# Kernel optimization log

Hardware: AMD Instinct MI355X
Metric: run time of the kernel (lower is better)

## Reference

```python
import jax, jax.numpy as jnp
import numpy as np

HEAD_SIZE = 64
N_EMBD = 768

def setup_inputs() -> dict:
    key = jax.random.key(0)
    kx, kq, kk, kv = jax.random.split(key, 4)
    x = jax.random.normal(kx, (4, 4096, N_EMBD), dtype=jnp.float32)
    s = 1.0 / np.sqrt(N_EMBD)
    Wq = jax.random.normal(kq, (N_EMBD, HEAD_SIZE), dtype=jnp.float32) * s
    Wk = jax.random.normal(kk, (N_EMBD, HEAD_SIZE), dtype=jnp.float32) * s
    Wv = jax.random.normal(kv, (N_EMBD, HEAD_SIZE), dtype=jnp.float32) * s
    return {"x": x, "Wq": Wq, "Wk": Wk, "Wv": Wv}

def reference(x, Wq, Wk, Wv):
    b, t, c = x.shape
    h = Wq.shape[1]
    q = jnp.einsum('btc,ch->bth', x, Wq)
    k = jnp.einsum('btc,ch->bth', x, Wk)
    v = jnp.einsum('btc,ch->bth', x, Wv)
    scores = jnp.einsum('bqh,bkh->bqk', q, k) / jnp.sqrt(jnp.float32(h))
    causal = jnp.tril(jnp.ones((t, t), dtype=bool))  # [t,t]
    scores = jnp.where(causal, scores, -jnp.inf)
    attn = jax.nn.softmax(scores, axis=-1)
    return jnp.einsum('bqk,bkh->bqh', attn, v)
```

## Files before the change

kernel.cpp:

```cpp
#include <hip/hip_runtime.h>
#include <math.h>

#define BB 4
#define TT 4096
#define CC 768
#define HH 64
#define NN 192
#define LDP 72
#define GR 32
#define BKK 64

typedef __bf16 bf16x8 __attribute__((ext_vector_type(8)));
typedef float floatx4 __attribute__((ext_vector_type(4)));
typedef unsigned short u16x8 __attribute__((ext_vector_type(8)));

__device__ inline unsigned short f2bf(float f) {
    union { __bf16 b; unsigned short u; } v;
    v.b = (__bf16)f;
    return v.u;
}

__global__ __launch_bounds__(256) void wprep(const float* __restrict__ Wq,
                                             const float* __restrict__ Wk,
                                             const float* __restrict__ Wv,
                                             unsigned short* __restrict__ wtf) {
    const int idx = blockIdx.x * 256 + threadIdx.x;
    if (idx >= NN * CC) return;
    const int j = idx & 7;
    const int lane = (idx >> 3) & 63;
    const int rest = idx >> 9;
    const int kg = rest % 24;
    const int n_tile = rest / 24;
    const int c = kg * 32 + (lane >> 4) * 8 + j;
    const int n = n_tile * 16 + (lane & 15);
    const float* W = (n < 64) ? Wq : (n < 128) ? Wk : Wv;
    wtf[idx] = f2bf(W[c * HH + (n & 63)]);
}

__global__ __launch_bounds__(256) void qkv_gemm(const float* __restrict__ x,
                                                const unsigned short* __restrict__ wtf,
                                                unsigned short* __restrict__ qb,
                                                unsigned short* __restrict__ kb,
                                                unsigned short* __restrict__ vbt) {
    __shared__ unsigned short As[GR * LDP];

    const int tid = threadIdx.x;
    const int w = tid >> 6, lane = tid & 63;
    const int l15 = lane & 15, quad = lane >> 4;
    const int m0 = blockIdx.x * GR;
    const int n0 = w * 48;
    const int nt0 = w * 3;

    const int ar = tid >> 3;
    const int akoff = (tid & 7) * 8;
    const float* xp = x + (size_t)(m0 + ar) * CC + akoff;

    floatx4 acc[2][3] = {};

    float4 pa0 = *(const float4*)(xp);
    float4 pa1 = *(const float4*)(xp + 4);

    for (int step = 0; step < 12; ++step) {
        __syncthreads();
        u16x8 pk;
        pk[0] = f2bf(pa0.x); pk[1] = f2bf(pa0.y);
        pk[2] = f2bf(pa0.z); pk[3] = f2bf(pa0.w);
        pk[4] = f2bf(pa1.x); pk[5] = f2bf(pa1.y);
        pk[6] = f2bf(pa1.z); pk[7] = f2bf(pa1.w);
        *(u16x8*)(As + ar * LDP + akoff) = pk;
        __syncthreads();

        if (step < 11) {
            pa0 = *(const float4*)(xp + (step + 1) * BKK);
            pa1 = *(const float4*)(xp + (step + 1) * BKK + 4);
        }

        bf16x8 a0[2], a1[2];
#pragma unroll
        for (int rg = 0; rg < 2; ++rg) {
            a0[rg] = *(const bf16x8*)(As + (16 * rg + l15) * LDP + quad * 8);
            a1[rg] = *(const bf16x8*)(As + (16 * rg + l15) * LDP + 32 + quad * 8);
        }
#pragma unroll
        for (int j = 0; j < 3; ++j) {
            const unsigned short* bp =
                wtf + ((size_t)((nt0 + j) * 24 + 2 * step) * 64 + lane) * 8;
            const bf16x8 b0 = *(const bf16x8*)(bp);
            const bf16x8 b1 = *(const bf16x8*)(bp + 512);
#pragma unroll
            for (int rg = 0; rg < 2; ++rg) {
                acc[rg][j] = __builtin_amdgcn_mfma_f32_16x16x32_bf16(a0[rg], b0, acc[rg][j], 0, 0, 0);
                acc[rg][j] = __builtin_amdgcn_mfma_f32_16x16x32_bf16(a1[rg], b1, acc[rg][j], 0, 0, 0);
            }
        }
    }

    const int b = m0 >> 12;
#pragma unroll
    for (int j = 0; j < 3; ++j) {
        const int n = n0 + j * 16 + l15;
        const int mid = n >> 6;
        const int h = n & 63;
#pragma unroll
        for (int rg = 0; rg < 2; ++rg) {
            const int tloc = (m0 & (TT - 1)) + 16 * rg + quad * 4;
            if (mid == 2) {
                ushort4 pk;
                pk.x = f2bf(acc[rg][j][0]); pk.y = f2bf(acc[rg][j][1]);
                pk.z = f2bf(acc[rg][j][2]); pk.w = f2bf(acc[rg][j][3]);
                *(ushort4*)(vbt + ((size_t)b * HH + h) * TT + tloc) = pk;
            } else {
                unsigned short* dst = (mid == 0) ? qb : kb;
#pragma unroll
                for (int r = 0; r < 4; ++r)
                    dst[(size_t)(m0 + 16 * rg + quad * 4 + r) * HH + h] = f2bf(acc[rg][j][r]);
            }
        }
    }
}

template<int CH>
__global__ __launch_bounds__(256) void attn_part(const unsigned short* __restrict__ qb,
                                                 const unsigned short* __restrict__ kb,
                                                 const unsigned short* __restrict__ vbt,
                                                 float* __restrict__ Opart,
                                                 float* __restrict__ lsum) {
    __shared__ unsigned short Ks[64 * LDP];
    __shared__ unsigned short VTs[64 * LDP];
    __shared__ unsigned short Ps[4][16 * LDP];

    constexpr int NG = 64 / CH;
    constexpr int TOTB = CH * (NG * (NG + 1)) / 2;

    const int b = blockIdx.x & 3;
    int rem = TOTB - 1 - (blockIdx.x >> 2);
    int g = 0;
    while (rem >= CH * (g + 1)) { rem -= CH * (g + 1); ++g; }
    const int qt = g * CH + rem / (g + 1);
    const int ch = rem - (rem / (g + 1)) * (g + 1);

    const int q0  = qt * 64;
    const int tid = threadIdx.x;
    const int w = tid >> 6, lane = tid & 63;
    const int l15 = lane & 15, quad = lane >> 4;

    const unsigned short* Qb  = qb  + (size_t)b * TT * HH;
    const unsigned short* Kb  = kb  + (size_t)b * TT * HH;
    const unsigned short* VTb = vbt + (size_t)b * HH * TT;

    const int qrow = q0 + 16 * w + l15;
    const bf16x8 qf0 = *(const bf16x8*)(Qb + (size_t)qrow * HH + quad * 8);
    const bf16x8 qf1 = *(const bf16x8*)(Qb + (size_t)qrow * HH + 32 + quad * 8);

    floatx4 O[4] = {};
    floatx4 lacc = {0.f, 0.f, 0.f, 0.f};

    const int kt0 = ch * CH;
    const int kt1 = min(kt0 + CH, qt + 1);
    for (int kt = kt0; kt < kt1; ++kt) {
        __syncthreads();
        const unsigned short* Kt = Kb + (size_t)(kt * 64) * HH;
        const unsigned short* Vt = VTb + kt * 64;
#pragma unroll
        for (int e = 0; e < 2; ++e) {
            const int chunk = tid + 256 * e;
            const int r = chunk >> 3, c0 = (chunk & 7) * 8;
            *(u16x8*)(Ks + r * LDP + c0)  = *(const u16x8*)(Kt + r * HH + c0);
            *(u16x8*)(VTs + r * LDP + c0) = *(const u16x8*)(Vt + (size_t)r * TT + c0);
        }
        __syncthreads();

        floatx4 s[4];
#pragma unroll
        for (int ki = 0; ki < 4; ++ki) {
            const bf16x8 kf0 = *(const bf16x8*)(Ks + (16 * ki + l15) * LDP + quad * 8);
            const bf16x8 kf1 = *(const bf16x8*)(Ks + (16 * ki + l15) * LDP + 32 + quad * 8);
            floatx4 c = {};
            c = __builtin_amdgcn_mfma_f32_16x16x32_bf16(qf0, kf0, c, 0, 0, 0);
            c = __builtin_amdgcn_mfma_f32_16x16x32_bf16(qf1, kf1, c, 0, 0, 0);
            s[ki] = c * 0.125f;
        }

        if (kt == qt) {
#pragma unroll
            for (int ki = 0; ki < 4; ++ki)
#pragma unroll
                for (int r = 0; r < 4; ++r) {
                    const int kloc = 16 * ki + l15;
                    const int qloc = 16 * w + quad * 4 + r;
                    if (kloc > qloc) s[ki][r] = -INFINITY;
                }
        }

#pragma unroll
        for (int ki = 0; ki < 4; ++ki)
#pragma unroll
            for (int r = 0; r < 4; ++r) {
                const float p = __expf(s[ki][r]);
                s[ki][r] = p;
                lacc[r] += p;
            }

        unsigned short* Pw = Ps[w];
#pragma unroll
        for (int ki = 0; ki < 4; ++ki)
#pragma unroll
            for (int r = 0; r < 4; ++r)
                Pw[(quad * 4 + r) * LDP + 16 * ki + l15] = f2bf(s[ki][r]);

        const bf16x8 pf0 = *(const bf16x8*)(Pw + l15 * LDP + quad * 8);
        const bf16x8 pf1 = *(const bf16x8*)(Pw + l15 * LDP + 32 + quad * 8);
#pragma unroll
        for (int di = 0; di < 4; ++di) {
            const bf16x8 vf0 = *(const bf16x8*)(VTs + (16 * di + l15) * LDP + quad * 8);
            const bf16x8 vf1 = *(const bf16x8*)(VTs + (16 * di + l15) * LDP + 32 + quad * 8);
            O[di] = __builtin_amdgcn_mfma_f32_16x16x32_bf16(pf0, vf0, O[di], 0, 0, 0);
            O[di] = __builtin_amdgcn_mfma_f32_16x16x32_bf16(pf1, vf1, O[di], 0, 0, 0);
        }
    }

    float l_r[4];
#pragma unroll
    for (int r = 0; r < 4; ++r) {
        float v = lacc[r];
#pragma unroll
        for (int msk = 8; msk >= 1; msk >>= 1) v += __shfl_xor(v, msk, 64);
        l_r[r] = v;
    }

    const int pbase = ((b * 64 + qt) * NG + ch) * 64;
    float* Op = Opart + (size_t)pbase * HH + 16 * w * HH;
#pragma unroll
    for (int di = 0; di < 4; ++di)
#pragma unroll
        for (int r = 0; r < 4; ++r)
            Op[(quad * 4 + r) * HH + 16 * di + l15] = O[di][r];
    if (l15 == 0) {
#pragma unroll
        for (int r = 0; r < 4; ++r)
            lsum[pbase + 16 * w + quad * 4 + r] = l_r[r];
    }
}

template<int CH>
__global__ __launch_bounds__(256) void attn_merge(const float* __restrict__ Opart,
                                                  const float* __restrict__ lsum,
                                                  float* __restrict__ out) {
    constexpr int NG = 64 / CH;
    const int g = blockIdx.x * 256 + threadIdx.x;
    const int row = g >> 6, d = g & 63;
    const int b = row >> 12, t = row & (TT - 1);
    const int qt = t >> 6, rloc = t & 63;
    const int nchunk = qt / CH + 1;
    const int pbase = ((b * 64 + qt) * NG) * 64 + rloc;

    float O = 0.f, L = 0.f;
#pragma unroll 4
    for (int c = 0; c < nchunk; ++c) {
        const int idx = pbase + c * 64;
        L += lsum[idx];
        O += Opart[(size_t)idx * HH + d];
    }
    out[(size_t)row * HH + d] = O / L;
}

__global__ __launch_bounds__(256) void attn_full(const unsigned short* __restrict__ qb,
                                                 const unsigned short* __restrict__ kb,
                                                 const unsigned short* __restrict__ vbt,
                                                 float* __restrict__ out) {
    __shared__ unsigned short Ks[64 * LDP];
    __shared__ unsigned short VTs[64 * LDP];
    __shared__ unsigned short Ps[4][16 * LDP];

    const int b   = blockIdx.x >> 6;
    const int qt  = blockIdx.x & 63;
    const int q0  = qt * 64;
    const int tid = threadIdx.x;
    const int w = tid >> 6, lane = tid & 63;
    const int l15 = lane & 15, quad = lane >> 4;

    const unsigned short* Qb  = qb  + (size_t)b * TT * HH;
    const unsigned short* Kb  = kb  + (size_t)b * TT * HH;
    const unsigned short* VTb = vbt + (size_t)b * HH * TT;

    const int qrow = q0 + 16 * w + l15;
    const bf16x8 qf0 = *(const bf16x8*)(Qb + (size_t)qrow * HH + quad * 8);
    const bf16x8 qf1 = *(const bf16x8*)(Qb + (size_t)qrow * HH + 32 + quad * 8);

    floatx4 O[4] = {};
    floatx4 lacc = {0.f, 0.f, 0.f, 0.f};

    for (int kt = 0; kt <= qt; ++kt) {
        __syncthreads();
        const unsigned short* Kt = Kb + (size_t)(kt * 64) * HH;
        const unsigned short* Vt = VTb + kt * 64;
#pragma unroll
        for (int e = 0; e < 2; ++e) {
            const int chunk = tid + 256 * e;
            const int r = chunk >> 3, c0 = (chunk & 7) * 8;
            *(u16x8*)(Ks + r * LDP + c0)  = *(const u16x8*)(Kt + r * HH + c0);
            *(u16x8*)(VTs + r * LDP + c0) = *(const u16x8*)(Vt + (size_t)r * TT + c0);
        }
        __syncthreads();

        floatx4 s[4];
#pragma unroll
        for (int ki = 0; ki < 4; ++ki) {
            const bf16x8 kf0 = *(const bf16x8*)(Ks + (16 * ki + l15) * LDP + quad * 8);
            const bf16x8 kf1 = *(const bf16x8*)(Ks + (16 * ki + l15) * LDP + 32 + quad * 8);
            floatx4 c = {};
            c = __builtin_amdgcn_mfma_f32_16x16x32_bf16(qf0, kf0, c, 0, 0, 0);
            c = __builtin_amdgcn_mfma_f32_16x16x32_bf16(qf1, kf1, c, 0, 0, 0);
            s[ki] = c * 0.125f;
        }
        if (kt == qt) {
#pragma unroll
            for (int ki = 0; ki < 4; ++ki)
#pragma unroll
                for (int r = 0; r < 4; ++r)
                    if (16 * ki + l15 > 16 * w + quad * 4 + r) s[ki][r] = -INFINITY;
        }
#pragma unroll
        for (int ki = 0; ki < 4; ++ki)
#pragma unroll
            for (int r = 0; r < 4; ++r) {
                const float p = __expf(s[ki][r]);
                s[ki][r] = p; lacc[r] += p;
            }

        unsigned short* Pw = Ps[w];
#pragma unroll
        for (int ki = 0; ki < 4; ++ki)
#pragma unroll
            for (int r = 0; r < 4; ++r)
                Pw[(quad * 4 + r) * LDP + 16 * ki + l15] = f2bf(s[ki][r]);

        const bf16x8 pf0 = *(const bf16x8*)(Pw + l15 * LDP + quad * 8);
        const bf16x8 pf1 = *(const bf16x8*)(Pw + l15 * LDP + 32 + quad * 8);
#pragma unroll
        for (int di = 0; di < 4; ++di) {
            const bf16x8 vf0 = *(const bf16x8*)(VTs + (16 * di + l15) * LDP + quad * 8);
            const bf16x8 vf1 = *(const bf16x8*)(VTs + (16 * di + l15) * LDP + 32 + quad * 8);
            O[di] = __builtin_amdgcn_mfma_f32_16x16x32_bf16(pf0, vf0, O[di], 0, 0, 0);
            O[di] = __builtin_amdgcn_mfma_f32_16x16x32_bf16(pf1, vf1, O[di], 0, 0, 0);
        }
    }
    float l_r[4];
#pragma unroll
    for (int r = 0; r < 4; ++r) {
        float v = lacc[r];
#pragma unroll
        for (int msk = 8; msk >= 1; msk >>= 1) v += __shfl_xor(v, msk, 64);
        l_r[r] = v;
    }
    float* outp = out + ((size_t)b * TT + q0 + 16 * w) * HH;
#pragma unroll
    for (int di = 0; di < 4; ++di)
#pragma unroll
        for (int r = 0; r < 4; ++r)
            outp[(quad * 4 + r) * HH + 16 * di + l15] = O[di][r] / l_r[r];
}

extern "C" void kernel_launch(void* const* d_in, const int* in_sizes, int n_in,
                              void* d_out, int out_size, void* d_ws, size_t ws_size,
                              hipStream_t stream) {
    const float* x  = (const float*)d_in[0];
    const float* Wq = (const float*)d_in[1];
    const float* Wk = (const float*)d_in[2];
    const float* Wv = (const float*)d_in[3];
    float* out = (float*)d_out;

    const size_t nQKV = (size_t)BB * TT * HH;
    unsigned short* qb  = (unsigned short*)d_ws;
    unsigned short* kb  = qb + nQKV;
    unsigned short* vbt = kb + nQKV;
    unsigned short* wtf = vbt + nQKV;
    float* Opart = (float*)(wtf + (size_t)NN * CC);

    const size_t prows8  = (size_t)BB * 64 * 8 * 64;
    const size_t prows16 = (size_t)BB * 64 * 4 * 64;
    float* lsum8  = Opart + prows8 * HH;
    float* lsum16 = Opart + prows16 * HH;
    const size_t need8  = (size_t)((char*)(lsum8  + prows8)  - (char*)d_ws);
    const size_t need16 = (size_t)((char*)(lsum16 + prows16) - (char*)d_ws);

    wprep<<<(NN * CC + 255) / 256, 256, 0, stream>>>(Wq, Wk, Wv, wtf);
    qkv_gemm<<<(BB * TT) / GR, 256, 0, stream>>>(x, wtf, qb, kb, vbt);
    if (ws_size >= need8) {
        attn_part<8><<<BB * 288, 256, 0, stream>>>(qb, kb, vbt, Opart, lsum8);
        attn_merge<8><<<(BB * TT * HH) / 256, 256, 0, stream>>>(Opart, lsum8, out);
    } else if (ws_size >= need16) {
        attn_part<16><<<BB * 160, 256, 0, stream>>>(qb, kb, vbt, Opart, lsum16);
        attn_merge<16><<<(BB * TT * HH) / 256, 256, 0, stream>>>(Opart, lsum16, out);
    } else {
        attn_full<<<BB * (TT / 64), 256, 0, stream>>>(qb, kb, vbt, out);
    }
}
```

Before: 131.9 us.

## Stage full x rows in LDS, bf16 partials, exp2 softmax, direct-write single-chunk tiles

The QKV GEMM now loads the whole 32x768 x tile into LDS once, so the per-step double sync is gone. Attention partial outputs are stored as bf16 instead of fp32, halving partial traffic. Softmax uses exp2 with the log2e constant folded into the scale. Query tiles that have only one chunk write normalized output directly and skip the merge. The merge kernel is vectorized to 8 elements per thread. In exchange, bf16 partials cost accuracy and the larger LDS footprint may reduce GEMM occupancy.

```diff
diff --git a/kernel.cpp b/kernel.cpp
--- a/kernel.cpp
+++ b/kernel.cpp
@@ -8,7 +8,8 @@
 #define NN 192
 #define LDP 72
 #define GR 32
-#define BKK 64
+#define XSTR 776
+#define SC2 0.180336880f
 
 typedef __bf16 bf16x8 __attribute__((ext_vector_type(8)));
 typedef float floatx4 __attribute__((ext_vector_type(4)));
@@ -18,6 +19,11 @@
     union { __bf16 b; unsigned short u; } v;
     v.b = (__bf16)f;
     return v.u;
+}
+__device__ inline float bf2f(unsigned short u) {
+    union { unsigned int u; float f; } v;
+    v.u = (unsigned int)u << 16;
+    return v.f;
 }
 
 __global__ __launch_bounds__(256) void wprep(const float* __restrict__ Wq,
@@ -42,7 +48,7 @@
                                                 unsigned short* __restrict__ qb,
                                                 unsigned short* __restrict__ kb,
                                                 unsigned short* __restrict__ vbt) {
-    __shared__ unsigned short As[GR * LDP];
+    __shared__ unsigned short As[GR * XSTR];
 
     const int tid = threadIdx.x;
     const int w = tid >> 6, lane = tid & 63;
@@ -51,35 +57,29 @@
     const int n0 = w * 48;
     const int nt0 = w * 3;
 
-    const int ar = tid >> 3;
-    const int akoff = (tid & 7) * 8;
-    const float* xp = x + (size_t)(m0 + ar) * CC + akoff;
+    const float* xbase = x + (size_t)m0 * CC;
+#pragma unroll
+    for (int e = 0; e < 12; ++e) {
+        const int c = tid + 256 * e;
+        const int r = c / 96, off = (c - r * 96) * 8;
+        const float4 v0 = *(const float4*)(xbase + (size_t)c * 8);
+        const float4 v1 = *(const float4*)(xbase + (size_t)c * 8 + 4);
+        u16x8 pk;
+        pk[0] = f2bf(v0.x); pk[1] = f2bf(v0.y); pk[2] = f2bf(v0.z); pk[3] = f2bf(v0.w);
+        pk[4] = f2bf(v1.x); pk[5] = f2bf(v1.y); pk[6] = f2bf(v1.z); pk[7] = f2bf(v1.w);
+        *(u16x8*)(As + r * XSTR + off) = pk;
+    }
+    __syncthreads();
 
     floatx4 acc[2][3] = {};
-
-    float4 pa0 = *(const float4*)(xp);
-    float4 pa1 = *(const float4*)(xp + 4);
-
+#pragma unroll 4
     for (int step = 0; step < 12; ++step) {
-        __syncthreads();
-        u16x8 pk;
-        pk[0] = f2bf(pa0.x); pk[1] = f2bf(pa0.y);
-        pk[2] = f2bf(pa0.z); pk[3] = f2bf(pa0.w);
-        pk[4] = f2bf(pa1.x); pk[5] = f2bf(pa1.y);
-        pk[6] = f2bf(pa1.z); pk[7] = f2bf(pa1.w);
-        *(u16x8*)(As + ar * LDP + akoff) = pk;
-        __syncthreads();
-
-        if (step < 11) {
-            pa0 = *(const float4*)(xp + (step + 1) * BKK);
-            pa1 = *(const float4*)(xp + (step + 1) * BKK + 4);
-        }
-
         bf16x8 a0[2], a1[2];
 #pragma unroll
         for (int rg = 0; rg < 2; ++rg) {
-            a0[rg] = *(const bf16x8*)(As + (16 * rg + l15) * LDP + quad * 8);
-            a1[rg] = *(const bf16x8*)(As + (16 * rg + l15) * LDP + 32 + quad * 8);
+            const unsigned short* ap = As + (16 * rg + l15) * XSTR + step * 64 + quad * 8;
+            a0[rg] = *(const bf16x8*)(ap);
+            a1[rg] = *(const bf16x8*)(ap + 32);
         }
 #pragma unroll
         for (int j = 0; j < 3; ++j) {
@@ -123,8 +123,9 @@
 __global__ __launch_bounds__(256) void attn_part(const unsigned short* __restrict__ qb,
                                                  const unsigned short* __restrict__ kb,
                                                  const unsigned short* __restrict__ vbt,
-                                                 float* __restrict__ Opart,
-                                                 float* __restrict__ lsum) {
+                                                 unsigned short* __restrict__ Opart,
+                                                 float* __restrict__ lsum,
+                                                 float* __restrict__ out) {
     __shared__ unsigned short Ks[64 * LDP];
     __shared__ unsigned short VTs[64 * LDP];
     __shared__ unsigned short Ps[4][16 * LDP];
@@ -178,7 +179,7 @@
             floatx4 c = {};
             c = __builtin_amdgcn_mfma_f32_16x16x32_bf16(qf0, kf0, c, 0, 0, 0);
             c = __builtin_amdgcn_mfma_f32_16x16x32_bf16(qf1, kf1, c, 0, 0, 0);
-            s[ki] = c * 0.125f;
+            s[ki] = c * SC2;
         }
 
         if (kt == qt) {
@@ -196,7 +197,7 @@
         for (int ki = 0; ki < 4; ++ki)
 #pragma unroll
             for (int r = 0; r < 4; ++r) {
-                const float p = __expf(s[ki][r]);
+                const float p = exp2f(s[ki][r]);
                 s[ki][r] = p;
                 lacc[r] += p;
             }
@@ -228,13 +229,23 @@
         l_r[r] = v;
     }
 
+    if (qt < CH) {
+        float* outp = out + ((size_t)b * TT + q0 + 16 * w) * HH;
+#pragma unroll
+        for (int di = 0; di < 4; ++di)
+#pragma unroll
+            for (int r = 0; r < 4; ++r)
+                outp[(quad * 4 + r) * HH + 16 * di + l15] = O[di][r] / l_r[r];
+        return;
+    }
+
     const int pbase = ((b * 64 + qt) * NG + ch) * 64;
-    float* Op = Opart + (size_t)pbase * HH + 16 * w * HH;
+    unsigned short* Op = Opart + (size_t)pbase * HH + 16 * w * HH;
 #pragma unroll
     for (int di = 0; di < 4; ++di)
 #pragma unroll
         for (int r = 0; r < 4; ++r)
-            Op[(quad * 4 + r) * HH + 16 * di + l15] = O[di][r];
+            Op[(quad * 4 + r) * HH + 16 * di + l15] = f2bf(O[di][r]);
     if (l15 == 0) {
 #pragma unroll
         for (int r = 0; r < 4; ++r)
@@ -243,25 +254,35 @@
 }
 
 template<int CH>
-__global__ __launch_bounds__(256) void attn_merge(const float* __restrict__ Opart,
+__global__ __launch_bounds__(256) void attn_merge(const unsigned short* __restrict__ Opart,
                                                   const float* __restrict__ lsum,
                                                   float* __restrict__ out) {
     constexpr int NG = 64 / CH;
     const int g = blockIdx.x * 256 + threadIdx.x;
-    const int row = g >> 6, d = g & 63;
+    const int row = g >> 3, oct = g & 7;
     const int b = row >> 12, t = row & (TT - 1);
     const int qt = t >> 6, rloc = t & 63;
+    if (qt < CH) return;
     const int nchunk = qt / CH + 1;
     const int pbase = ((b * 64 + qt) * NG) * 64 + rloc;
-
-    float O = 0.f, L = 0.f;
-#pragma unroll 4
+    const int d0 = oct * 8;
+
+    float L = 0.f;
+    float a[8] = {};
     for (int c = 0; c < nchunk; ++c) {
         const int idx = pbase + c * 64;
         L += lsum[idx];
-        O += Opart[(size_t)idx * HH + d];
-    }
-    out[(size_t)row * HH + d] = O / L;
+        const u16x8 pv = *(const u16x8*)(Opart + (size_t)idx * HH + d0);
+#pragma unroll
+        for (int k = 0; k < 8; ++k) a[k] += bf2f(pv[k]);
+    }
+    const float inv = 1.f / L;
+    float4 o0, o1;
+    o0.x = a[0] * inv; o0.y = a[1] * inv; o0.z = a[2] * inv; o0.w = a[3] * inv;
+    o1.x = a[4] * inv; o1.y = a[5] * inv; o1.z = a[6] * inv; o1.w = a[7] * inv;
+    float* dst = out + (size_t)row * HH + d0;
+    *(float4*)(dst) = o0;
+    *(float4*)(dst + 4) = o1;
 }
 
 __global__ __launch_bounds__(256) void attn_full(const unsigned short* __restrict__ qb,
@@ -311,7 +332,7 @@
             floatx4 c = {};
             c = __builtin_amdgcn_mfma_f32_16x16x32_bf16(qf0, kf0, c, 0, 0, 0);
             c = __builtin_amdgcn_mfma_f32_16x16x32_bf16(qf1, kf1, c, 0, 0, 0);
-            s[ki] = c * 0.125f;
+            s[ki] = c * SC2;
         }
         if (kt == qt) {
 #pragma unroll
@@ -324,7 +345,7 @@
         for (int ki = 0; ki < 4; ++ki)
 #pragma unroll
             for (int r = 0; r < 4; ++r) {
-                const float p = __expf(s[ki][r]);
+                const float p = exp2f(s[ki][r]);
                 s[ki][r] = p; lacc[r] += p;
             }
 
@@ -375,23 +396,23 @@
     unsigned short* kb  = qb + nQKV;
     unsigned short* vbt = kb + nQKV;
     unsigned short* wtf = vbt + nQKV;
-    float* Opart = (float*)(wtf + (size_t)NN * CC);
+    unsigned short* Opart = wtf + (size_t)NN * CC;
 
     const size_t prows8  = (size_t)BB * 64 * 8 * 64;
     const size_t prows16 = (size_t)BB * 64 * 4 * 64;
-    float* lsum8  = Opart + prows8 * HH;
-    float* lsum16 = Opart + prows16 * HH;
+    float* lsum8  = (float*)(Opart + prows8 * HH);
+    float* lsum16 = (float*)(Opart + prows16 * HH);
     const size_t need8  = (size_t)((char*)(lsum8  + prows8)  - (char*)d_ws);
     const size_t need16 = (size_t)((char*)(lsum16 + prows16) - (char*)d_ws);
 
     wprep<<<(NN * CC + 255) / 256, 256, 0, stream>>>(Wq, Wk, Wv, wtf);
     qkv_gemm<<<(BB * TT) / GR, 256, 0, stream>>>(x, wtf, qb, kb, vbt);
     if (ws_size >= need8) {
-        attn_part<8><<<BB * 288, 256, 0, stream>>>(qb, kb, vbt, Opart, lsum8);
-        attn_merge<8><<<(BB * TT * HH) / 256, 256, 0, stream>>>(Opart, lsum8, out);
+        attn_part<8><<<BB * 288, 256, 0, stream>>>(qb, kb, vbt, Opart, lsum8, out);
+        attn_merge<8><<<(BB * TT * 8) / 256, 256, 0, stream>>>(Opart, lsum8, out);
     } else if (ws_size >= need16) {
-        attn_part<16><<<BB * 160, 256, 0, stream>>>(qb, kb, vbt, Opart, lsum16);
-        attn_merge<16><<<(BB * TT * HH) / 256, 256, 0, stream>>>(Opart, lsum16, out);
+        attn_part<16><<<BB * 160, 256, 0, stream>>>(qb, kb, vbt, Opart, lsum16, out);
+        attn_merge<16><<<(BB * TT * 8) / 256, 256, 0, stream>>>(Opart, lsum16, out);
     } else {
         attn_full<<<BB * (TT / 64), 256, 0, stream>>>(qb, kb, vbt, out);
     }
```

Result: no change. 130.4 us (-1.1%).
